# Performance work log

Hardware: AMD Instinct MI355X
Metric: run time of the kernel (lower is better)

## Reference

```python
import jax, jax.numpy as jnp
import numpy as np

N = 50000
E = 500000
IN_C = 128
HEADS = 4
OUT_C = 64
EDGE_DIM = 32
NEG_SLOPE = 0.2  # PyG GATv2Conv default


def setup_inputs() -> dict:
    key = jax.random.key(0)
    ks = jax.random.split(key, 10)
    x = jax.random.normal(ks[0], (N, IN_C), dtype=jnp.float32)
    edge_index = jax.random.randint(ks[1], (2, E), 0, N, dtype=jnp.int64)
    edge_attr = jax.random.normal(ks[2], (E, EDGE_DIM), dtype=jnp.float32)
    s = 1.0 / np.sqrt(IN_C)
    W_l = jax.random.normal(ks[3], (IN_C, HEADS * OUT_C), dtype=jnp.float32) * s
    b_l = jnp.zeros((HEADS * OUT_C,), dtype=jnp.float32)
    W_r = jax.random.normal(ks[4], (IN_C, HEADS * OUT_C), dtype=jnp.float32) * s
    b_r = jnp.zeros((HEADS * OUT_C,), dtype=jnp.float32)
    W_e = jax.random.normal(ks[5], (EDGE_DIM, HEADS * OUT_C), dtype=jnp.float32) / np.sqrt(EDGE_DIM)
    att = jax.random.normal(ks[6], (HEADS, OUT_C), dtype=jnp.float32) / np.sqrt(OUT_C)
    bias = jnp.zeros((OUT_C,), dtype=jnp.float32)
    return {"x": x, "edge_index": edge_index, "edge_attr": edge_attr,
            "W_l": W_l, "b_l": b_l, "W_r": W_r, "b_r": b_r,
            "W_e": W_e, "att": att, "bias": bias}


def reference(x, edge_index, edge_attr, W_l, b_l, W_r, b_r, W_e, att, bias):
    # GATv2Conv forward (eval mode: dropout inactive), concat=False -> mean over heads
    src, dst = edge_index[0], edge_index[1]  # edge j -> i (source_to_target)
    x_l = (x @ W_l + b_l).reshape(N, HEADS, OUT_C)  # source transform
    x_r = (x @ W_r + b_r).reshape(N, HEADS, OUT_C)  # target transform
    e = (edge_attr @ W_e).reshape(E, HEADS, OUT_C)
    # per-edge score: att . LeakyReLU(x_l[j] + x_r[i] + e)
    m = x_l[src] + x_r[dst] + e                      # [E, H, C]
    m = jnp.where(m > 0, m, NEG_SLOPE * m)
    alpha = jnp.einsum('ehc,hc->eh', m, att)         # [E, H]
    # softmax over incoming edges of each target node
    amax = jax.ops.segment_max(alpha, dst, num_segments=N)   # [N, H]
    alpha = jnp.exp(alpha - amax[dst])
    denom = jax.ops.segment_sum(alpha, dst, num_segments=N)  # [N, H]
    alpha = alpha / denom[dst]
    # scatter-add weighted source messages
    out = jax.ops.segment_sum(alpha[:, :, None] * x_l[src], dst, num_segments=N)  # [N, H, C]
    out = out.mean(axis=1) + bias                    # concat=False -> mean heads
    return out
```

## Files before the change

kernel.cpp:

```cpp
#include <hip/hip_runtime.h>
#include <cstddef>

#define Nn 50000
#define Ee 500000
#define INC 128
#define HC 256
#define OUTC 64
#define EDIM 32
#define NEG 0.2f
#define NB 196
#define GEMMB 782

typedef __attribute__((ext_vector_type(8))) short short8;
typedef __attribute__((ext_vector_type(4))) float f32x4;

__device__ __forceinline__ unsigned short f2bf(float f) {
    unsigned u = __float_as_uint(f);
    return (unsigned short)((u + 0x7FFFu + ((u >> 16) & 1u)) >> 16);
}
__device__ __forceinline__ float bf2f(unsigned short v) {
    return __uint_as_float(((unsigned)v) << 16);
}

__device__ __forceinline__ float row_sum16(float x) {
    int i;
    i = __builtin_amdgcn_mov_dpp(__float_as_int(x), 0xB1, 0xF, 0xF, true);
    x += __int_as_float(i);
    i = __builtin_amdgcn_mov_dpp(__float_as_int(x), 0x4E, 0xF, 0xF, true);
    x += __int_as_float(i);
    i = __builtin_amdgcn_mov_dpp(__float_as_int(x), 0x141, 0xF, 0xF, true);
    x += __int_as_float(i);
    i = __builtin_amdgcn_mov_dpp(__float_as_int(x), 0x140, 0xF, 0xF, true);
    x += __int_as_float(i);
    return x;
}

__global__ __launch_bounds__(256) void pack_kernel(
    const float* __restrict__ Wl, const float* __restrict__ Wr,
    const float* __restrict__ We,
    unsigned short* __restrict__ wlf, unsigned short* __restrict__ wrf,
    unsigned short* __restrict__ wef, int* __restrict__ deg)
{
    int sid = blockIdx.x * 256 + threadIdx.x;
    if (sid >= 9216) {
        int i = sid - 9216;
        if (i < Nn) deg[i] = 0;
        return;
    }
    const float* W; unsigned short* dst; int s; int col; int k0;
    if (sid < 8192) {
        if (sid < 4096) { W = Wl; dst = wlf; s = sid; }
        else            { W = Wr; dst = wrf; s = sid - 4096; }
        int lane = s & 63;
        int T    = (s >> 6) & 15;
        int kc   = s >> 10;
        col = (lane & 15) * 16 + T;
        k0  = kc * 32 + (lane >> 4) * 8;
    } else {
        W = We; dst = wef; s = sid - 8192;
        int lane = s & 63;
        int nt   = (s >> 6) & 3;
        int cb   = s >> 8;
        col = cb * 64 + (lane & 15) * 4 + nt;
        k0  = (lane >> 4) * 8;
    }
    unsigned short tmp[8];
    #pragma unroll
    for (int j = 0; j < 8; ++j) tmp[j] = f2bf(W[(size_t)(k0 + j) * HC + col]);
    *(uint4*)(dst + (size_t)s * 8) = *(uint4*)tmp;
}

__global__ __launch_bounds__(256) void gemm_hist_kernel(
    const float* __restrict__ X,
    const unsigned short* __restrict__ wlf, const float* __restrict__ bl,
    const unsigned short* __restrict__ wrf, const float* __restrict__ br,
    unsigned short* __restrict__ Ylb, unsigned short* __restrict__ Yrb,
    const int* __restrict__ ei, int* __restrict__ deg)
{
    if (blockIdx.x >= GEMMB) {
        int e = (blockIdx.x - GEMMB) * 256 + threadIdx.x;
        if (e < Ee) atomicAdd(deg + ei[Ee + e], 1);
        return;
    }

    const int tid = threadIdx.x, lane = tid & 63;
    const int l15 = lane & 15, l4 = lane >> 4;
    const int r0 = blockIdx.x * 64 + (tid >> 6) * 16;

    int arow = r0 + l15; if (arow >= Nn) arow = Nn - 1;
    short8 af[4];
    #pragma unroll
    for (int kc = 0; kc < 4; ++kc) {
        const f32x4* p = (const f32x4*)(X + (size_t)arow * INC + kc * 32 + l4 * 8);
        f32x4 v0 = p[0], v1 = p[1];
        short8 a;
        a[0]=(short)f2bf(v0.x); a[1]=(short)f2bf(v0.y); a[2]=(short)f2bf(v0.z); a[3]=(short)f2bf(v0.w);
        a[4]=(short)f2bf(v1.x); a[5]=(short)f2bf(v1.y); a[6]=(short)f2bf(v1.z); a[7]=(short)f2bf(v1.w);
        af[kc] = a;
    }

    #pragma unroll 1
    for (int w = 0; w < 2; ++w) {
        const unsigned short* wf = w ? wrf : wlf;
        const float* b = w ? br : bl;
        unsigned short* Yb = w ? Yrb : Ylb;

        f32x4 acc[16];
        #pragma unroll
        for (int T = 0; T < 16; ++T) acc[T] = (f32x4){0.f, 0.f, 0.f, 0.f};

        #pragma unroll
        for (int kc = 0; kc < 4; ++kc) {
            #pragma unroll
            for (int T = 0; T < 16; ++T) {
                short8 bf = *(const short8*)(wf + ((size_t)(kc * 16 + T) * 64 + lane) * 8);
                acc[T] = __builtin_amdgcn_mfma_f32_16x16x32_bf16(af[kc], bf, acc[T], 0, 0, 0);
            }
        }

        float bb[16];
        #pragma unroll
        for (int t4 = 0; t4 < 4; ++t4) {
            float4 v = *(const float4*)(b + l15 * 16 + t4 * 4);
            bb[t4*4+0]=v.x; bb[t4*4+1]=v.y; bb[t4*4+2]=v.z; bb[t4*4+3]=v.w;
        }

        #pragma unroll
        for (int r = 0; r < 4; ++r) {
            int orow = r0 + l4 * 4 + r;
            if (orow < Nn) {
                unsigned short o[16];
                #pragma unroll
                for (int T = 0; T < 16; ++T) o[T] = f2bf(acc[T][r] + bb[T]);
                *(uint4*)(Yb + (size_t)orow * HC + l15 * 16)     = *(uint4*)(o);
                *(uint4*)(Yb + (size_t)orow * HC + l15 * 16 + 8) = *(uint4*)(o + 8);
            }
        }
    }
}

__global__ __launch_bounds__(256) void scan1_kernel(
    const int* __restrict__ deg, int* __restrict__ off, int* __restrict__ bsum) {
    __shared__ int s[256];
    int i = blockIdx.x * 256 + threadIdx.x;
    int v = (i < Nn) ? deg[i] : 0;
    s[threadIdx.x] = v;
    __syncthreads();
    #pragma unroll
    for (int d = 1; d < 256; d <<= 1) {
        int t = (threadIdx.x >= d) ? s[threadIdx.x - d] : 0;
        __syncthreads();
        s[threadIdx.x] += t;
        __syncthreads();
    }
    if (i < Nn) off[i] = s[threadIdx.x] - v;
    if (threadIdx.x == 255) bsum[blockIdx.x] = s[255];
}
__global__ __launch_bounds__(256) void scan3_kernel(
    int* __restrict__ off, const int* __restrict__ bsum, int* __restrict__ cur) {
    __shared__ int s[256];
    int t = threadIdx.x;
    int v = (t < NB) ? bsum[t] : 0;
    s[t] = v;
    __syncthreads();
    #pragma unroll
    for (int d = 1; d < 256; d <<= 1) {
        int tv = (t >= d) ? s[t - d] : 0;
        __syncthreads();
        s[t] += tv;
        __syncthreads();
    }
    int base = (blockIdx.x == 0) ? 0 : s[blockIdx.x - 1];
    int i = blockIdx.x * 256 + t;
    if (i < Nn) {
        int o = off[i] + base;
        off[i] = o;
        cur[i] = o;
    }
}
__global__ __launch_bounds__(256) void scatter_kernel(
    const int* __restrict__ ei, int* __restrict__ cur,
    int* __restrict__ csr_e, int* __restrict__ csr_s) {
    int e = blockIdx.x * 256 + threadIdx.x;
    if (e >= Ee) return;
    int d = ei[Ee + e];
    int pos = atomicAdd(cur + d, 1);
    csr_e[pos] = e;
    csr_s[pos] = ei[e];
}

__global__ __launch_bounds__(256) void fused_node_kernel(
    const unsigned short* __restrict__ xlb, const unsigned short* __restrict__ xrb,
    const int* __restrict__ csr_e, const int* __restrict__ csr_s,
    const float* __restrict__ ea, const unsigned short* __restrict__ wef,
    const float* __restrict__ att, const int* __restrict__ off,
    const int* __restrict__ deg, const float* __restrict__ bias,
    float* __restrict__ out)
{
    __shared__ unsigned short cache[4][16][256];
    __shared__ float sAl[4][64];
    __shared__ float shw[4][64];
    const int lane = threadIdx.x & 63;
    const int wv   = threadIdx.x >> 6;
    const int l15  = lane & 15, l4 = lane >> 4;
    const int n    = blockIdx.x * 4 + wv;
    if (n >= Nn) return;

    const int start = off[n];
    const int len   = deg[n];

    if (len == 0) {
        if (lane < 16) {
            float4 b4 = *(const float4*)(bias + lane * 4);
            *(float4*)(out + (size_t)n * OUTC + lane * 4) = b4;
        }
        return;
    }

    const int sA   = (l15 & 3) * 4 + (l15 >> 2);
    const int eidx = lane >> 2;
    const int hagg = lane >> 4;

    float m = -3.4e38f, d = 0.f;
    float4 acc = make_float4(0.f, 0.f, 0.f, 0.f);

    for (int c0 = 0; c0 < len; c0 += 16) {
        const int cl   = (len - c0 < 16) ? (len - c0) : 16;
        const int rmax = (cl + 3) >> 2;

        short8 afrag;
        {
            int sc_ = (sA < cl) ? sA : (cl - 1);
            int e = csr_e[start + c0 + sc_];
            const f32x4* pp = (const f32x4*)(ea + (size_t)e * EDIM + l4 * 8);
            f32x4 v0 = __builtin_nontemporal_load(pp);
            f32x4 v1 = __builtin_nontemporal_load(pp + 1);
            afrag[0]=(short)f2bf(v0.x); afrag[1]=(short)f2bf(v0.y);
            afrag[2]=(short)f2bf(v0.z); afrag[3]=(short)f2bf(v0.w);
            afrag[4]=(short)f2bf(v1.x); afrag[5]=(short)f2bf(v1.y);
            afrag[6]=(short)f2bf(v1.z); afrag[7]=(short)f2bf(v1.w);
        }

        unsigned soff[4];
        #pragma unroll
        for (int r = 0; r < 4; ++r) {
            int slot = r * 4 + l4;
            int sc_ = (slot < cl) ? slot : (cl - 1);
            soff[r] = (unsigned)csr_s[start + c0 + sc_] * (unsigned)HC;
        }

        #pragma unroll 1
        for (int cb = 0; cb < 4; ++cb) {
            f32x4 acc4[4];
            const f32x4 z = {0.f, 0.f, 0.f, 0.f};
            #pragma unroll
            for (int nt = 0; nt < 4; ++nt) {
                short8 bfrag = *(const short8*)(wef + ((size_t)(cb * 4 + nt) * 64 + lane) * 8);
                acc4[nt] = __builtin_amdgcn_mfma_f32_16x16x32_bf16(afrag, bfrag, z, 0, 0, 0);
            }

            const unsigned cc = (unsigned)(cb * 64 + l15 * 4);
            ushort4 gr4 = *(const ushort4*)(xrb + (size_t)n * HC + cc);
            float xr0 = bf2f(gr4.x), xr1 = bf2f(gr4.y);
            float xr2 = bf2f(gr4.z), xr3 = bf2f(gr4.w);
            float4 atv = *(const float4*)(att + cc);

            #pragma unroll
            for (int r = 0; r < 4; ++r) {
                if (r < rmax) {
                    int slot = r * 4 + l4;
                    ushort4 gl4 = *(const ushort4*)(xlb + soff[r] + cc);
                    *(ushort4*)(&cache[wv][slot][cc]) = gl4;
                    float m0 = acc4[0][r] + bf2f(gl4.x) + xr0;
                    float m1 = acc4[1][r] + bf2f(gl4.y) + xr1;
                    float m2 = acc4[2][r] + bf2f(gl4.z) + xr2;
                    float m3 = acc4[3][r] + bf2f(gl4.w) + xr3;
                    m0 = fmaxf(m0, NEG * m0);
                    m1 = fmaxf(m1, NEG * m1);
                    m2 = fmaxf(m2, NEG * m2);
                    m3 = fmaxf(m3, NEG * m3);
                    float p;
                    p = atv.x * m0;
                    p = fmaf(atv.y, m1, p);
                    p = fmaf(atv.z, m2, p);
                    p = fmaf(atv.w, m3, p);
                    p = row_sum16(p);
                    if (l15 == 0) sAl[wv][slot * 4 + cb] = p;
                }
            }
        }

        float a = (eidx < cl) ? sAl[wv][lane] : -3.4e38f;
        float cm = a;
        cm = fmaxf(cm, __shfl_xor(cm, 4, 64));
        cm = fmaxf(cm, __shfl_xor(cm, 8, 64));
        cm = fmaxf(cm, __shfl_xor(cm, 16, 64));
        cm = fmaxf(cm, __shfl_xor(cm, 32, 64));
        float mn = fmaxf(m, cm);
        float sc = __expf(m - mn);
        float w  = (eidx < cl) ? __expf(a - mn) : 0.f;
        float ws = w;
        ws += __shfl_xor(ws, 4, 64);
        ws += __shfl_xor(ws, 8, 64);
        ws += __shfl_xor(ws, 16, 64);
        ws += __shfl_xor(ws, 32, 64);
        d = d * sc + ws;
        m = mn;
        shw[wv][lane] = w;
        float sca = __shfl(sc, hagg, 64);
        acc.x *= sca; acc.y *= sca; acc.z *= sca; acc.w *= sca;
        #pragma unroll 4
        for (int i = 0; i < cl; ++i) {
            float wi = shw[wv][i * 4 + hagg];
            ushort4 g = *(const ushort4*)(&cache[wv][i][lane * 4]);
            acc.x = fmaf(wi, bf2f(g.x), acc.x);
            acc.y = fmaf(wi, bf2f(g.y), acc.y);
            acc.z = fmaf(wi, bf2f(g.z), acc.z);
            acc.w = fmaf(wi, bf2f(g.w), acc.w);
        }
    }

    float dh = __shfl(d, hagg, 64);
    float di = 1.f / dh;
    float4 r;
    r.x = acc.x * di; r.y = acc.y * di; r.z = acc.z * di; r.w = acc.w * di;
    r.x += __shfl_xor(r.x, 16, 64); r.y += __shfl_xor(r.y, 16, 64);
    r.z += __shfl_xor(r.z, 16, 64); r.w += __shfl_xor(r.w, 16, 64);
    r.x += __shfl_xor(r.x, 32, 64); r.y += __shfl_xor(r.y, 32, 64);
    r.z += __shfl_xor(r.z, 32, 64); r.w += __shfl_xor(r.w, 32, 64);
    if (lane < 16) {
        float4 b4 = *(const float4*)(bias + lane * 4);
        float4 o = make_float4(b4.x + 0.25f * r.x, b4.y + 0.25f * r.y,
                               b4.z + 0.25f * r.z, b4.w + 0.25f * r.w);
        *(float4*)(out + (size_t)n * OUTC + lane * 4) = o;
    }
}

extern "C" void kernel_launch(void* const* d_in, const int* in_sizes, int n_in,
                              void* d_out, int out_size, void* d_ws, size_t ws_size,
                              hipStream_t stream)
{
    const float* x    = (const float*)d_in[0];
    const int*   ei   = (const int*)d_in[1];
    const float* ea   = (const float*)d_in[2];
    const float* Wl   = (const float*)d_in[3];
    const float* bl   = (const float*)d_in[4];
    const float* Wr   = (const float*)d_in[5];
    const float* br   = (const float*)d_in[6];
    const float* We   = (const float*)d_in[7];
    const float* att  = (const float*)d_in[8];
    const float* bias = (const float*)d_in[9];
    float* out = (float*)d_out;

    unsigned short* xlb   = (unsigned short*)d_ws;
    unsigned short* xrb   = xlb + (size_t)Nn * HC;
    unsigned short* wef   = xrb + (size_t)Nn * HC;
    unsigned short* wlf   = wef + 8192;
    unsigned short* wrf   = wlf + 32768;
    int*            deg   = (int*)(wrf + 32768);
    int*            off   = deg + Nn;
    int*            cur   = off + Nn;
    int*            bsum  = cur + Nn;
    int*            csr_e = bsum + 256;
    int*            csr_s = csr_e + Ee;

    pack_kernel<<<232, 256, 0, stream>>>(Wl, Wr, We, wlf, wrf, wef, deg);
    gemm_hist_kernel<<<GEMMB + (Ee + 255) / 256, 256, 0, stream>>>(
        x, wlf, bl, wrf, br, xlb, xrb, ei, deg);
    scan1_kernel<<<NB, 256, 0, stream>>>(deg, off, bsum);
    scan3_kernel<<<NB, 256, 0, stream>>>(off, bsum, cur);
    scatter_kernel<<<(Ee + 255) / 256, 256, 0, stream>>>(ei, cur, csr_e, csr_s);
    fused_node_kernel<<<(Nn + 3) / 4, 256, 0, stream>>>(
        xlb, xrb, csr_e, csr_s, ea, wef, att, off, deg, bias, out);
}
```

Measured before the change: 257.0 us.

## Halve per-iteration edge chunk to 8 and pack score math into float2

Each node's incoming edges are now processed in chunks of 8 instead of 16. This halves the shared-memory neighbour cache and the score buffers, and drops one shuffle step from the max and sum reductions. The intent is to cut LDS footprint so more wavefronts fit per CU, and to skip unused slots for low-degree nodes. In exchange, nodes with more than 8 in-edges take extra loop iterations, and each iteration repeats the edge-feature MFMAs and the online-softmax rescale. The LeakyReLU and attention dot product are also rewritten with 2-wide float vectors to encourage packed FP32 instructions.

After: 294.3 us. +14.5%, slower.

```diff
diff --git a/kernel.cpp b/kernel.cpp
--- a/kernel.cpp
+++ b/kernel.cpp
@@ -13,6 +13,7 @@
 
 typedef __attribute__((ext_vector_type(8))) short short8;
 typedef __attribute__((ext_vector_type(4))) float f32x4;
+typedef __attribute__((ext_vector_type(2))) float f32x2;
 
 __device__ __forceinline__ unsigned short f2bf(float f) {
     unsigned u = __float_as_uint(f);
@@ -197,9 +198,9 @@
     const int* __restrict__ deg, const float* __restrict__ bias,
     float* __restrict__ out)
 {
-    __shared__ unsigned short cache[4][16][256];
-    __shared__ float sAl[4][64];
-    __shared__ float shw[4][64];
+    __shared__ unsigned short cache[4][8][256];
+    __shared__ float sAl[4][32];
+    __shared__ float shw[4][32];
     const int lane = threadIdx.x & 63;
     const int wv   = threadIdx.x >> 6;
     const int l15  = lane & 15, l4 = lane >> 4;
@@ -224,8 +225,8 @@
     float m = -3.4e38f, d = 0.f;
     float4 acc = make_float4(0.f, 0.f, 0.f, 0.f);
 
-    for (int c0 = 0; c0 < len; c0 += 16) {
-        const int cl   = (len - c0 < 16) ? (len - c0) : 16;
+    for (int c0 = 0; c0 < len; c0 += 8) {
+        const int cl   = (len - c0 < 8) ? (len - c0) : 8;
         const int rmax = (cl + 3) >> 2;
 
         short8 afrag;
@@ -241,9 +242,9 @@
             afrag[6]=(short)f2bf(v1.z); afrag[7]=(short)f2bf(v1.w);
         }
 
-        unsigned soff[4];
-        #pragma unroll
-        for (int r = 0; r < 4; ++r) {
+        unsigned soff[2];
+        #pragma unroll
+        for (int r = 0; r < 2; ++r) {
             int slot = r * 4 + l4;
             int sc_ = (slot < cl) ? slot : (cl - 1);
             soff[r] = (unsigned)csr_s[start + c0 + sc_] * (unsigned)HC;
@@ -261,41 +262,39 @@
 
             const unsigned cc = (unsigned)(cb * 64 + l15 * 4);
             ushort4 gr4 = *(const ushort4*)(xrb + (size_t)n * HC + cc);
-            float xr0 = bf2f(gr4.x), xr1 = bf2f(gr4.y);
-            float xr2 = bf2f(gr4.z), xr3 = bf2f(gr4.w);
+            f32x2 gr01 = {bf2f(gr4.x), bf2f(gr4.y)};
+            f32x2 gr23 = {bf2f(gr4.z), bf2f(gr4.w)};
             float4 atv = *(const float4*)(att + cc);
+            f32x2 at01 = {atv.x, atv.y};
+            f32x2 at23 = {atv.z, atv.w};
 
             #pragma unroll
-            for (int r = 0; r < 4; ++r) {
+            for (int r = 0; r < 2; ++r) {
                 if (r < rmax) {
                     int slot = r * 4 + l4;
                     ushort4 gl4 = *(const ushort4*)(xlb + soff[r] + cc);
                     *(ushort4*)(&cache[wv][slot][cc]) = gl4;
-                    float m0 = acc4[0][r] + bf2f(gl4.x) + xr0;
-                    float m1 = acc4[1][r] + bf2f(gl4.y) + xr1;
-                    float m2 = acc4[2][r] + bf2f(gl4.z) + xr2;
-                    float m3 = acc4[3][r] + bf2f(gl4.w) + xr3;
-                    m0 = fmaxf(m0, NEG * m0);
-                    m1 = fmaxf(m1, NEG * m1);
-                    m2 = fmaxf(m2, NEG * m2);
-                    m3 = fmaxf(m3, NEG * m3);
-                    float p;
-                    p = atv.x * m0;
-                    p = fmaf(atv.y, m1, p);
-                    p = fmaf(atv.z, m2, p);
-                    p = fmaf(atv.w, m3, p);
+                    f32x2 m01 = {acc4[0][r], acc4[1][r]};
+                    f32x2 m23 = {acc4[2][r], acc4[3][r]};
+                    f32x2 gl01 = {bf2f(gl4.x), bf2f(gl4.y)};
+                    f32x2 gl23 = {bf2f(gl4.z), bf2f(gl4.w)};
+                    m01 = m01 + gl01 + gr01;
+                    m23 = m23 + gl23 + gr23;
+                    m01 = __builtin_elementwise_max(m01, m01 * NEG);
+                    m23 = __builtin_elementwise_max(m23, m23 * NEG);
+                    f32x2 pf = at01 * m01 + at23 * m23;
+                    float p = pf.x + pf.y;
                     p = row_sum16(p);
                     if (l15 == 0) sAl[wv][slot * 4 + cb] = p;
                 }
             }
         }
 
-        float a = (eidx < cl) ? sAl[wv][lane] : -3.4e38f;
+        float a = (eidx < cl) ? sAl[wv][lane & 31] : -3.4e38f;
         float cm = a;
         cm = fmaxf(cm, __shfl_xor(cm, 4, 64));
         cm = fmaxf(cm, __shfl_xor(cm, 8, 64));
         cm = fmaxf(cm, __shfl_xor(cm, 16, 64));
-        cm = fmaxf(cm, __shfl_xor(cm, 32, 64));
         float mn = fmaxf(m, cm);
         float sc = __expf(m - mn);
         float w  = (eidx < cl) ? __expf(a - mn) : 0.f;
@@ -303,10 +302,9 @@
         ws += __shfl_xor(ws, 4, 64);
         ws += __shfl_xor(ws, 8, 64);
         ws += __shfl_xor(ws, 16, 64);
-        ws += __shfl_xor(ws, 32, 64);
         d = d * sc + ws;
         m = mn;
-        shw[wv][lane] = w;
+        if (lane < 32) shw[wv][lane] = w;
         float sca = __shfl(sc, hagg, 64);
         acc.x *= sca; acc.y *= sca; acc.z *= sca; acc.w *= sca;
         #pragma unroll 4
```
